# Kernel tuning notes

Hardware: AMD Instinct MI355X
Metric: run time of the kernel (lower is better)

## Reference

```python
import jax, jax.numpy as jnp
import numpy as np

B, T, D = 8, 1024, 1024
KD, VD, H = 1024, 1024, 16  # key_dim_total, value_dim_total, num_heads
NEG = -1e9
EPS = 1e-5


def setup_inputs() -> dict:
    key = jax.random.key(0)
    ks = jax.random.split(key, 8)
    x = jax.random.normal(ks[0], (B, T, D), dtype=jnp.float32)
    x_lens = jax.random.randint(ks[1], (B,), 1, T + 1).astype(jnp.int32)
    ln_gamma = jnp.ones((D,), jnp.float32)
    ln_beta = jnp.zeros((D,), jnp.float32)
    qkv_out = 2 * KD + VD
    w_qkv = jax.random.normal(ks[2], (D, qkv_out), jnp.float32) / np.sqrt(D)
    b_qkv = jax.random.normal(ks[3], (qkv_out,), jnp.float32) * 0.01
    w_out = jax.random.normal(ks[4], (VD, D), jnp.float32) / np.sqrt(VD)
    b_out = jax.random.normal(ks[5], (D,), jnp.float32) * 0.01
    return {"x": x, "x_lens": x_lens, "ln_gamma": ln_gamma, "ln_beta": ln_beta,
            "w_qkv": w_qkv, "b_qkv": b_qkv, "w_out": w_out, "b_out": b_out}


def reference(x, x_lens, ln_gamma, ln_beta, w_qkv, b_qkv, w_out, b_out):
    # LayerNorm over feature dim
    mu = jnp.mean(x, axis=-1, keepdims=True)
    var = jnp.mean(jnp.square(x - mu), axis=-1, keepdims=True)
    xn = (x - mu) * jax.lax.rsqrt(var + EPS) * ln_gamma + ln_beta
    # fused QKV projection
    qkv = xn @ w_qkv + b_qkv  # (B, T, 2*KD+VD)
    q, k, v = qkv[..., :KD], qkv[..., KD:2 * KD], qkv[..., 2 * KD:]
    hd = KD // H
    q = q.reshape(B, T, H, hd).transpose(0, 2, 1, 3)  # (B,H,T,hd)
    k = k.reshape(B, T, H, hd).transpose(0, 2, 1, 3)
    v = v.reshape(B, T, H, VD // H).transpose(0, 2, 1, 3)
    scale = 1.0 / np.sqrt(hd)
    scores = jnp.einsum("bhtd,bhsd->bhts", q, k) * scale  # (B,H,T,T)
    # combined causal + kv-length padding mask (additive in original; boolean here)
    causal = jnp.tril(jnp.ones((T, T), bool))  # (T,T)
    kv_valid = jnp.arange(T)[None, :] < x_lens[:, None]  # (B,T)
    mask = causal[None, None, :, :] & kv_valid[:, None, None, :]
    scores = jnp.where(mask, scores, NEG)
    att = jax.nn.softmax(scores, axis=-1)
    att_out = jnp.einsum("bhts,bhsd->bhtd", att, v)  # (B,H,T,hd_v)
    out = att_out.transpose(0, 2, 1, 3).reshape(B, T, VD)
    out = out @ w_out + b_out
    return out
```

## Files before the change

### kernel.cpp

```cpp
#include <hip/hip_runtime.h>

#define D_MODEL 1024
#define T_SEQ   1024
#define BATCH   8
#define NHEAD   16
#define HDIM    64

typedef float      v4f   __attribute__((ext_vector_type(4)));
typedef _Float16   half8 __attribute__((ext_vector_type(8)));
typedef _Float16   half4h __attribute__((ext_vector_type(4)));
typedef unsigned int ui4 __attribute__((ext_vector_type(4)));

__device__ __forceinline__ void load_lds16(const _Float16* g, _Float16* l) {
  __builtin_amdgcn_global_load_lds(
      (const __attribute__((address_space(1))) unsigned int*)g,
      (__attribute__((address_space(3))) unsigned int*)l, 16, 0, 0);
}

__global__ __launch_bounds__(256) void ln_kernel(const float* __restrict__ x,
                                                 const float* __restrict__ gamma,
                                                 const float* __restrict__ beta,
                                                 _Float16* __restrict__ xn) {
  int row = blockIdx.x;
  int tid = threadIdx.x;
  const float* xr = x + (size_t)row * D_MODEL;
  v4f xv = *(const v4f*)(xr + tid * 4);
  float s  = xv[0] + xv[1] + xv[2] + xv[3];
  float sq = xv[0]*xv[0] + xv[1]*xv[1] + xv[2]*xv[2] + xv[3]*xv[3];
#pragma unroll
  for (int off = 32; off > 0; off >>= 1) {
    s  += __shfl_xor(s, off);
    sq += __shfl_xor(sq, off);
  }
  __shared__ float ps[4], psq[4];
  int wave = tid >> 6;
  if ((tid & 63) == 0) { ps[wave] = s; psq[wave] = sq; }
  __syncthreads();
  float tot  = ps[0] + ps[1] + ps[2] + ps[3];
  float totq = psq[0] + psq[1] + psq[2] + psq[3];
  float mean = tot * (1.0f / D_MODEL);
  float var  = totq * (1.0f / D_MODEL) - mean * mean;
  float rs   = rsqrtf(var + 1e-5f);
  v4f gv = *(const v4f*)(gamma + tid * 4);
  v4f bv = *(const v4f*)(beta + tid * 4);
  half4h o;
#pragma unroll
  for (int i = 0; i < 4; ++i)
    o[i] = (_Float16)((xv[i] - mean) * rs * gv[i] + bv[i]);
  *(half4h*)(xn + (size_t)row * D_MODEL + tid * 4) = o;
}

__global__ __launch_bounds__(256) void fragize_kernel(const float* __restrict__ W,
                                                      _Float16* __restrict__ Bf,
                                                      int N, int K) {
  int g = blockIdx.x * 256 + threadIdx.x;
  int lane = g & 63, tile = g >> 6;
  int ktiles = K >> 5;
  int kt = tile % ktiles, nt = tile / ktiles;
  int n  = nt * 16 + (lane & 15);
  int k0 = kt * 32 + (lane >> 4) * 8;
  half8 o;
#pragma unroll
  for (int j = 0; j < 8; ++j) o[j] = (_Float16)W[(size_t)(k0 + j) * N + n];
  *(half8*)(Bf + (size_t)g * 8) = o;
}

__global__ __launch_bounds__(256) void vtrans_kernel(const _Float16* __restrict__ Vd,
                                                     _Float16* __restrict__ Vt) {
  __shared__ _Float16 tile[64][68];
  int p  = blockIdx.y;
  int t0 = blockIdx.x * 64;
  int tid = threadIdx.x;
  int r = tid >> 3, c = (tid & 7) * 8;
#pragma unroll
  for (int it = 0; it < 2; ++it) {
    int rr = r + it * 32;
    *(ui4*)&tile[rr][c] = *(const ui4*)&Vd[((size_t)p * T_SEQ + t0 + rr) * HDIM + c];
  }
  __syncthreads();
#pragma unroll
  for (int it = 0; it < 2; ++it) {
    int d = r + it * 32;
    half8 o;
#pragma unroll
    for (int j = 0; j < 8; ++j) o[j] = tile[c + j][d];
    *(half8*)&Vt[((size_t)p * HDIM + d) * T_SEQ + t0 + c] = o;
  }
}

template <int MODE>
__global__ __launch_bounds__(256) void gemm_kernel(
    const _Float16* __restrict__ A, const _Float16* __restrict__ Bfrag,
    const float* __restrict__ bias, int M, int N, int K,
    float* __restrict__ outF,
    _Float16* __restrict__ Qd, _Float16* __restrict__ Kd, _Float16* __restrict__ Vd) {
  __shared__ _Float16 As[2][128 * 32];
  int tid = threadIdx.x;
  int wave = tid >> 6, lane = tid & 63;
  int l15 = lane & 15, quad = lane >> 4;
  int wm = (wave & 1) * 64, wn = (wave >> 1) * 64;
  int m0 = blockIdx.x * 128, n0 = blockIdx.y * 128;
  v4f zero = {0.f, 0.f, 0.f, 0.f};
  v4f acc[4][4];
#pragma unroll
  for (int i = 0; i < 4; ++i)
#pragma unroll
    for (int j = 0; j < 4; ++j) acc[i][j] = zero;

  int ar0 = tid >> 2;
  int akc = (tid & 3) * 8;
  const _Float16* Ap = A + (size_t)(m0 + ar0) * K + akc;
  _Float16* AsW0 = &As[0][0] + wave * 512;
  _Float16* AsW1 = &As[1][0] + wave * 512;
  const int ktiles = K >> 5;
  const _Float16* Bp = Bfrag + (size_t)((n0 + wn) >> 4) * ktiles * 512 + lane * 8;

  load_lds16(Ap, AsW0);
  load_lds16(Ap + (size_t)64 * K, AsW0 + 2048);
  for (int kt = 0; kt < ktiles; ++kt) {
    int cur = kt & 1;
    __syncthreads();
    if (kt + 1 < ktiles) {
      _Float16* nx = cur ? AsW0 : AsW1;
      load_lds16(Ap + (kt + 1) * 32,                  nx);
      load_lds16(Ap + (kt + 1) * 32 + (size_t)64 * K, nx + 2048);
    }
    half8 bf[4];
#pragma unroll
    for (int ni = 0; ni < 4; ++ni)
      bf[ni] = *(const half8*)(Bp + ((size_t)ni * ktiles + kt) * 512);
    half8 af[4];
#pragma unroll
    for (int i = 0; i < 4; ++i)
      af[i] = *(const half8*)&As[cur][(wm + i * 16 + l15) * 32 + quad * 8];
#pragma unroll
    for (int mi = 0; mi < 4; ++mi)
#pragma unroll
      for (int ni = 0; ni < 4; ++ni)
        acc[mi][ni] = __builtin_amdgcn_mfma_f32_16x16x32_f16(af[mi], bf[ni], acc[mi][ni], 0, 0, 0);
  }
  float bv[4];
#pragma unroll
  for (int ni = 0; ni < 4; ++ni) bv[ni] = bias[n0 + wn + ni * 16 + l15];
#pragma unroll
  for (int mi = 0; mi < 4; ++mi) {
#pragma unroll
    for (int ni = 0; ni < 4; ++ni) {
      int n = n0 + wn + ni * 16 + l15;
#pragma unroll
      for (int r = 0; r < 4; ++r) {
        int m = m0 + wm + mi * 16 + quad * 4 + r;
        float v = acc[mi][ni][r] + bv[ni];
        if (MODE == 1) {
          outF[(size_t)m * N + n] = v;
        } else {
          int b = m >> 10, t = m & 1023;
          int h = (n >> 6) & 15, d = n & 63;
          size_t idx = ((size_t)(b * NHEAD + h) * T_SEQ + t) * HDIM + d;
          if (n < 1024)        Qd[idx] = (_Float16)(v * 0.18033688f);
          else if (n < 2048)   Kd[idx] = (_Float16)v;
          else                 Vd[idx] = (_Float16)v;
        }
      }
    }
  }
}

__global__ __launch_bounds__(256) void attn_kernel(const _Float16* __restrict__ Qg,
                                                   const _Float16* __restrict__ Kk,
                                                   const _Float16* __restrict__ Vt,
                                                   const int* __restrict__ x_lens,
                                                   _Float16* __restrict__ att) {
  __shared__ _Float16 Ks[2][64 * 32];
  __shared__ _Float16 Vs[2][64 * 32];
  __shared__ _Float16 Pb[4][16 * 72];
  int blk = blockIdx.x;
  int qt = blk >> 7;
  int bh = blk & 127;
  int h  = bh & 15;
  int b  = bh >> 4;
  int t0 = qt * 64;
  int len = x_lens[b];
  int tid = threadIdx.x;
  int wave = tid >> 6, lane = tid & 63;
  int l15 = lane & 15, quad = lane >> 4;
  size_t plane = (size_t)(b * NHEAD + h) * (T_SEQ * HDIM);
  int qrow = t0 + wave * 16;
  int qabs = qrow + l15;
  const _Float16* Qp = Qg + plane + (size_t)qabs * HDIM + quad * 8;
  half8 qf0 = *(const half8*)Qp;
  half8 qf1 = *(const half8*)(Qp + 32);
  v4f zero = {0.f, 0.f, 0.f, 0.f};
  float m_i = -1e30f, l_i = 0.f;
  v4f Ov[4];
#pragma unroll
  for (int nt = 0; nt < 4; ++nt) Ov[nt] = zero;

  int jmaxb = min(t0 + 63, len - 1);
  int ntile = (jmaxb >> 6) + 1;
  int wjmax = min(qrow + 15, len - 1);

  const _Float16* src[4];
  _Float16* dst[4];
  int strd[4];
#pragma unroll
  for (int i = 0; i < 4; ++i) {
    int u = wave * 4 + i;
    int q = u & 3, hf = (u >> 2) & 1;
    if (u < 8) {
      src[i] = Kk + plane + (size_t)(q * 16 + (lane >> 2)) * HDIM + hf * 32 + (lane & 3) * 8;
      dst[i] = &Ks[hf][0] + q * 512;
      strd[i] = 64 * HDIM;
    } else {
      src[i] = Vt + plane + (size_t)(q * 16 + (lane >> 2)) * T_SEQ + hf * 32 + (lane & 3) * 8;
      dst[i] = &Vs[hf][0] + q * 512;
      strd[i] = 64;
    }
  }

  for (int jt = 0; jt < ntile; ++jt) {
    int j0 = jt * 64;
    __syncthreads();
#pragma unroll
    for (int i = 0; i < 4; ++i) {
      load_lds16(src[i], dst[i]);
      src[i] += strd[i];
    }
    __syncthreads();
    if (j0 <= wjmax) {
      v4f s[4];
#pragma unroll
      for (int nt = 0; nt < 4; ++nt) {
        s[nt] = zero;
        half8 k0 = *(const half8*)&Ks[0][(nt * 16 + l15) * 32 + quad * 8];
        half8 k1 = *(const half8*)&Ks[1][(nt * 16 + l15) * 32 + quad * 8];
        s[nt] = __builtin_amdgcn_mfma_f32_16x16x32_f16(k0, qf0, s[nt], 0, 0, 0);
        s[nt] = __builtin_amdgcn_mfma_f32_16x16x32_f16(k1, qf1, s[nt], 0, 0, 0);
      }
      float mnew = m_i;
      bool full = (j0 + 63 <= qrow) && (j0 + 63 < len);
      if (full) {
#pragma unroll
        for (int nt = 0; nt < 4; ++nt)
#pragma unroll
          for (int r = 0; r < 4; ++r)
            mnew = fmaxf(mnew, s[nt][r]);
      } else {
#pragma unroll
        for (int nt = 0; nt < 4; ++nt) {
#pragma unroll
          for (int r = 0; r < 4; ++r) {
            int key = j0 + nt * 16 + quad * 4 + r;
            float v = (key <= qabs && key < len) ? s[nt][r] : -1e30f;
            s[nt][r] = v;
            mnew = fmaxf(mnew, v);
          }
        }
      }
      mnew = fmaxf(mnew, __shfl_xor(mnew, 16));
      mnew = fmaxf(mnew, __shfl_xor(mnew, 32));
      float alpha = exp2f(m_i - mnew);
      m_i = mnew;
      float rsum = 0.f;
#pragma unroll
      for (int nt = 0; nt < 4; ++nt)
#pragma unroll
        for (int r = 0; r < 4; ++r) {
          float p = exp2f(s[nt][r] - mnew);
          s[nt][r] = p;
          rsum += p;
        }
      rsum += __shfl_xor(rsum, 16);
      rsum += __shfl_xor(rsum, 32);
      l_i = l_i * alpha + rsum;
#pragma unroll
      for (int nt = 0; nt < 4; ++nt)
#pragma unroll
        for (int r = 0; r < 4; ++r) Ov[nt][r] *= alpha;
#pragma unroll
      for (int nt = 0; nt < 4; ++nt) {
        half4h pk;
#pragma unroll
        for (int r = 0; r < 4; ++r) pk[r] = (_Float16)s[nt][r];
        *(half4h*)&Pb[wave][l15 * 72 + nt * 16 + quad * 4] = pk;
      }
      asm volatile("s_waitcnt lgkmcnt(0)" ::: "memory");
      half8 pf0 = *(const half8*)&Pb[wave][l15 * 72 + quad * 8];
      half8 pf1 = *(const half8*)&Pb[wave][l15 * 72 + 32 + quad * 8];
#pragma unroll
      for (int nt = 0; nt < 4; ++nt) {
        half8 v0 = *(const half8*)&Vs[0][(nt * 16 + l15) * 32 + quad * 8];
        half8 v1 = *(const half8*)&Vs[1][(nt * 16 + l15) * 32 + quad * 8];
        Ov[nt] = __builtin_amdgcn_mfma_f32_16x16x32_f16(v0, pf0, Ov[nt], 0, 0, 0);
        Ov[nt] = __builtin_amdgcn_mfma_f32_16x16x32_f16(v1, pf1, Ov[nt], 0, 0, 0);
      }
    }
  }
  float inv = 1.0f / l_i;
#pragma unroll
  for (int nt = 0; nt < 4; ++nt) {
    half4h ok;
#pragma unroll
    for (int r = 0; r < 4; ++r) ok[r] = (_Float16)(Ov[nt][r] * inv);
    *(half4h*)&Pb[wave][l15 * 72 + nt * 16 + quad * 4] = ok;
  }
  asm volatile("s_waitcnt lgkmcnt(0)" ::: "memory");
  int r0 = lane >> 3, c0 = (lane & 7) * 8;
  half8 o0 = *(const half8*)&Pb[wave][r0 * 72 + c0];
  half8 o1 = *(const half8*)&Pb[wave][(r0 + 8) * 72 + c0];
  *(half8*)&att[((size_t)(b * T_SEQ) + qrow + r0) * D_MODEL + h * HDIM + c0] = o0;
  *(half8*)&att[((size_t)(b * T_SEQ) + qrow + r0 + 8) * D_MODEL + h * HDIM + c0] = o1;
}

extern "C" void kernel_launch(void* const* d_in, const int* in_sizes, int n_in,
                              void* d_out, int out_size, void* d_ws, size_t ws_size,
                              hipStream_t stream) {
  const float* x        = (const float*)d_in[0];
  const int*   x_lens   = (const int*)d_in[1];
  const float* ln_gamma = (const float*)d_in[2];
  const float* ln_beta  = (const float*)d_in[3];
  const float* w_qkv    = (const float*)d_in[4];
  const float* b_qkv    = (const float*)d_in[5];
  const float* w_out    = (const float*)d_in[6];
  const float* b_out    = (const float*)d_in[7];
  float* out = (float*)d_out;

  char* w = (char*)d_ws;
  _Float16* xn    = (_Float16*)w; w += (size_t)8192 * 1024 * 2;
  _Float16* BfQKV = (_Float16*)w; w += (size_t)3072 * 1024 * 2;
  _Float16* BfOut = (_Float16*)w; w += (size_t)1024 * 1024 * 2;
  _Float16* Qd    = (_Float16*)w; w += (size_t)8192 * 1024 * 2;
  _Float16* Kd    = (_Float16*)w; w += (size_t)8192 * 1024 * 2;
  _Float16* Vd    = (_Float16*)w; w += (size_t)8192 * 1024 * 2;
  _Float16* att   = (_Float16*)w; w += (size_t)8192 * 1024 * 2;
  _Float16* Vt    = xn;

  fragize_kernel<<<(3072 * 1024 / 8) / 256, 256, 0, stream>>>(w_qkv, BfQKV, 3072, 1024);
  fragize_kernel<<<(1024 * 1024 / 8) / 256, 256, 0, stream>>>(w_out, BfOut, 1024, 1024);
  ln_kernel<<<8192, 256, 0, stream>>>(x, ln_gamma, ln_beta, xn);
  gemm_kernel<0><<<dim3(8192 / 128, 3072 / 128), 256, 0, stream>>>(
      xn, BfQKV, b_qkv, 8192, 3072, 1024, nullptr, Qd, Kd, Vd);
  vtrans_kernel<<<dim3(16, 128), 256, 0, stream>>>(Vd, Vt);
  attn_kernel<<<2048, 256, 0, stream>>>(Qd, Kd, Vt, x_lens, att);
  gemm_kernel<1><<<dim3(8192 / 128, 1024 / 128), 256, 0, stream>>>(
      att, BfOut, b_out, 8192, 1024, 1024, out, nullptr, nullptr, nullptr);
}
```

Baseline: 254.0 us.

## Replace QKV GEMM with 128x256-tile, 8-wave pipelined kernel using transposed weights

Swaps the QKV projection GEMM for a new 512-thread kernel that computes 128x256 output tiles. Both operands are staged through double-buffered, XOR-swizzled LDS with direct global-to-LDS loads, and MFMA phases are interleaved with barriers and wave priority changes. The weight is now pre-transposed into a K-contiguous fp16 layout by a new tiled transpose kernel, replacing the fragment layout. This aims to raise data reuse and overlap loads with MFMA, at the cost of higher LDS use, more barriers, and scattered scalar fp16 stores in the epilogue.

```diff
diff --git a/kernel.cpp b/kernel.cpp
--- a/kernel.cpp
+++ b/kernel.cpp
@@ -65,6 +65,35 @@
   *(half8*)(Bf + (size_t)g * 8) = o;
 }
 
+__global__ __launch_bounds__(256) void wtrans_kernel(const float* __restrict__ W,
+                                                     _Float16* __restrict__ Wt,
+                                                     int N, int K) {
+  __shared__ _Float16 t[64][72];
+  int k0 = blockIdx.x * 64, n0 = blockIdx.y * 64;
+  int tid = threadIdx.x;
+  int r = tid >> 3, c = (tid & 7) * 8;
+#pragma unroll
+  for (int it = 0; it < 2; ++it) {
+    int row = r + it * 32;
+    const float* src = W + (size_t)(k0 + row) * N + n0 + c;
+    v4f x0 = *(const v4f*)src;
+    v4f x1 = *(const v4f*)(src + 4);
+#pragma unroll
+    for (int j = 0; j < 4; ++j) t[row][c + j] = (_Float16)x0[j];
+#pragma unroll
+    for (int j = 0; j < 4; ++j) t[row][c + 4 + j] = (_Float16)x1[j];
+  }
+  __syncthreads();
+#pragma unroll
+  for (int it = 0; it < 2; ++it) {
+    int d = r + it * 32;
+    half8 o;
+#pragma unroll
+    for (int j = 0; j < 8; ++j) o[j] = t[c + j][d];
+    *(half8*)(Wt + (size_t)(n0 + d) * K + k0 + c) = o;
+  }
+}
+
 __global__ __launch_bounds__(256) void vtrans_kernel(const _Float16* __restrict__ Vd,
                                                      _Float16* __restrict__ Vt) {
   __shared__ _Float16 tile[64][68];
@@ -86,6 +115,124 @@
     for (int j = 0; j < 8; ++j) o[j] = tile[c + j][d];
     *(half8*)&Vt[((size_t)p * HDIM + d) * T_SEQ + t0 + c] = o;
   }
+}
+
+
+#define BAR   __builtin_amdgcn_s_barrier()
+#define LGKM0 asm volatile("s_waitcnt lgkmcnt(0)" ::: "memory")
+#define VMC2  asm volatile("s_waitcnt vmcnt(2)" ::: "memory")
+#define PRIO1 __builtin_amdgcn_s_setprio(1)
+#define PRIO0 __builtin_amdgcn_s_setprio(0)
+
+#define RDA(dst, BUF, KK)                                                       \
+  _Pragma("unroll")                                                             \
+  for (int d2 = 0; d2 < 4; ++d2)                                                \
+    dst[d2] = *(const half8*)(lds + (BUF) +                                     \
+                              (wm + d2 * 16 + l15) * 64 +                       \
+                              ((((KK) * 4 + quad) ^ swz) * 8));
+
+#define RDB(dst, BUF, NI0, KK)                                                  \
+  _Pragma("unroll")                                                             \
+  for (int n2 = 0; n2 < 2; ++n2)                                                \
+    dst[n2] = *(const half8*)(lds + (BUF) + 8192 +                              \
+                              (wn + ((NI0) + n2) * 16 + l15) * 64 +             \
+                              ((((KK) * 4 + quad) ^ swz) * 8));
+
+#define MFQ(A_, B_, NI0)                                                        \
+  _Pragma("unroll")                                                             \
+  for (int mi = 0; mi < 4; ++mi)                                                \
+    _Pragma("unroll")                                                           \
+    for (int n2 = 0; n2 < 2; ++n2)                                              \
+      acc[mi][(NI0) + n2] = __builtin_amdgcn_mfma_f32_16x16x32_f16(             \
+          A_[mi], B_[n2], acc[mi][(NI0) + n2], 0, 0, 0);
+
+#define STGA(BUF, R0, KT)                                                       \
+  load_lds16(Asrc + (size_t)(R0) * 1024 + (KT) * 64, ldst + (BUF) + (R0) * 64)
+#define STGB(BUF, R0, KT)                                                       \
+  load_lds16(Bsrc + (size_t)(R0) * 1024 + (KT) * 64, ldst + (BUF) + 8192 + (R0) * 64)
+
+__global__ __launch_bounds__(512, 2) void gemm256_qkv(
+    const _Float16* __restrict__ A, const _Float16* __restrict__ Bt,
+    const float* __restrict__ bias,
+    _Float16* __restrict__ Qd, _Float16* __restrict__ Kd, _Float16* __restrict__ Vd) {
+  __shared__ _Float16 lds[49152];
+  const int K = 1024;
+  int tid  = threadIdx.x;
+  int wave = tid >> 6, lane = tid & 63;
+  int l15  = lane & 15, quad = lane >> 4;
+  int wm = (wave & 1) * 64, wn = (wave >> 1) * 64;
+  int m0 = blockIdx.x * 128, n0 = blockIdx.y * 256;
+  int swz = l15 & 7;
+
+  int ric = tid >> 3;
+  int colofs = ((tid & 7) ^ (ric & 7)) * 8;
+  const _Float16* Asrc = A  + (size_t)(m0 + ric) * K + colofs;
+  const _Float16* Bsrc = Bt + (size_t)(n0 + ric) * K + colofs;
+  _Float16* ldst = lds + wave * 512;
+
+  const int B0 = 0, B1 = 24576;
+  v4f acc[4][4];
+  v4f zero = {0.f, 0.f, 0.f, 0.f};
+#pragma unroll
+  for (int i = 0; i < 4; ++i)
+#pragma unroll
+    for (int j = 0; j < 4; ++j) acc[i][j] = zero;
+
+  STGA(B0, 0, 0); STGA(B0, 64, 0);
+  STGB(B0, 0, 0); STGB(B0, 64, 0); STGB(B0, 128, 0); STGB(B0, 192, 0);
+  STGA(B1, 0, 1); STGA(B1, 64, 1);
+  VMC2; BAR;
+
+  half8 a0[4], a1[4], bl[2], bh[2];
+#pragma unroll 1
+  for (int i = 0; i < 8; ++i) {
+    int kt1 = 2 * i + 1;
+    int kt2 = (2 * i + 2 < 16) ? 2 * i + 2 : 15;
+    int kt3 = (2 * i + 3 < 16) ? 2 * i + 3 : 15;
+    RDA(a0, B0, 0); RDB(bl, B0, 0, 0);
+    STGB(B1, 0, kt1); STGB(B1, 64, kt1);
+    BAR; LGKM0; PRIO1; MFQ(a0, bl, 0); PRIO0; BAR;
+    RDB(bh, B0, 2, 0);
+    STGB(B1, 128, kt1); STGB(B1, 192, kt1);
+    BAR; LGKM0; PRIO1; MFQ(a0, bh, 2); PRIO0; BAR;
+    RDA(a1, B0, 1); RDB(bl, B0, 0, 1);
+    BAR; LGKM0; PRIO1; MFQ(a1, bl, 0); PRIO0; BAR;
+    RDB(bh, B0, 2, 1);
+    STGA(B0, 0, kt2); STGA(B0, 64, kt2);
+    VMC2; BAR; LGKM0; PRIO1; MFQ(a1, bh, 2); PRIO0; BAR;
+    RDA(a0, B1, 0); RDB(bl, B1, 0, 0);
+    STGB(B0, 0, kt2); STGB(B0, 64, kt2);
+    BAR; LGKM0; PRIO1; MFQ(a0, bl, 0); PRIO0; BAR;
+    RDB(bh, B1, 2, 0);
+    STGB(B0, 128, kt2); STGB(B0, 192, kt2);
+    BAR; LGKM0; PRIO1; MFQ(a0, bh, 2); PRIO0; BAR;
+    RDA(a1, B1, 1); RDB(bl, B1, 0, 1);
+    BAR; LGKM0; PRIO1; MFQ(a1, bl, 0); PRIO0; BAR;
+    RDB(bh, B1, 2, 1);
+    STGA(B1, 0, kt3); STGA(B1, 64, kt3);
+    VMC2; BAR; LGKM0; PRIO1; MFQ(a1, bh, 2); PRIO0; BAR;
+  }
+
+  float bv[4];
+#pragma unroll
+  for (int ni = 0; ni < 4; ++ni) bv[ni] = bias[n0 + wn + ni * 16 + l15];
+  int sec = n0 >> 10;
+  _Float16* dstP = sec == 0 ? Qd : (sec == 1 ? Kd : Vd);
+  float scale = sec == 0 ? 0.18033688f : 1.0f;
+#pragma unroll
+  for (int mi = 0; mi < 4; ++mi)
+#pragma unroll
+    for (int ni = 0; ni < 4; ++ni) {
+      int n = n0 + wn + ni * 16 + l15;
+      int h = (n >> 6) & 15, d = n & 63;
+#pragma unroll
+      for (int r = 0; r < 4; ++r) {
+        int m = m0 + wm + mi * 16 + quad * 4 + r;
+        int b = m >> 10, t = m & 1023;
+        float v = acc[mi][ni][r] + bv[ni];
+        dstP[((size_t)(b * NHEAD + h) * T_SEQ + t) * HDIM + d] = (_Float16)(v * scale);
+      }
+    }
 }
 
 template <int MODE>
@@ -327,7 +474,7 @@
 
   char* w = (char*)d_ws;
   _Float16* xn    = (_Float16*)w; w += (size_t)8192 * 1024 * 2;
-  _Float16* BfQKV = (_Float16*)w; w += (size_t)3072 * 1024 * 2;
+  _Float16* WtQKV = (_Float16*)w; w += (size_t)3072 * 1024 * 2;
   _Float16* BfOut = (_Float16*)w; w += (size_t)1024 * 1024 * 2;
   _Float16* Qd    = (_Float16*)w; w += (size_t)8192 * 1024 * 2;
   _Float16* Kd    = (_Float16*)w; w += (size_t)8192 * 1024 * 2;
@@ -335,11 +482,10 @@
   _Float16* att   = (_Float16*)w; w += (size_t)8192 * 1024 * 2;
   _Float16* Vt    = xn;
 
-  fragize_kernel<<<(3072 * 1024 / 8) / 256, 256, 0, stream>>>(w_qkv, BfQKV, 3072, 1024);
+  wtrans_kernel<<<dim3(16, 48), 256, 0, stream>>>(w_qkv, WtQKV, 3072, 1024);
   fragize_kernel<<<(1024 * 1024 / 8) / 256, 256, 0, stream>>>(w_out, BfOut, 1024, 1024);
   ln_kernel<<<8192, 256, 0, stream>>>(x, ln_gamma, ln_beta, xn);
-  gemm_kernel<0><<<dim3(8192 / 128, 3072 / 128), 256, 0, stream>>>(
-      xn, BfQKV, b_qkv, 8192, 3072, 1024, nullptr, Qd, Kd, Vd);
+  gemm256_qkv<<<dim3(64, 12), 512, 0, stream>>>(xn, WtQKV, b_qkv, Qd, Kd, Vd);
   vtrans_kernel<<<dim3(16, 128), 256, 0, stream>>>(Vd, Vt);
   attn_kernel<<<2048, 256, 0, stream>>>(Qd, Kd, Vt, x_lens, att);
   gemm_kernel<1><<<dim3(8192 / 128, 1024 / 128), 256, 0, stream>>>(
```

New measurement: 246.0 us. 3.1% less time.

## Double-buffer K/V tiles in attention and schedule heaviest query tiles first

Applied to the files above, without the earlier changes.

Attention K/V tiles now use two LDS buffers, so the next tile's global-to-LDS load is issued before computing on the current one, with vmcnt waits replacing the pair of full syncthreads. Query tiles are launched in reverse order so the longest causal blocks start first, and MFMA sections are wrapped with s_setprio to favour matrix issue. This hides load latency at the cost of double the K/V LDS, which may lower occupancy.

```diff
diff --git a/kernel.cpp b/kernel.cpp
--- a/kernel.cpp
+++ b/kernel.cpp
@@ -171,11 +171,11 @@
                                                    const _Float16* __restrict__ Vt,
                                                    const int* __restrict__ x_lens,
                                                    _Float16* __restrict__ att) {
-  __shared__ _Float16 Ks[2][64 * 32];
-  __shared__ _Float16 Vs[2][64 * 32];
+  __shared__ _Float16 Ks[2][2][2048];
+  __shared__ _Float16 Vs[2][2][2048];
   __shared__ _Float16 Pb[4][16 * 72];
   int blk = blockIdx.x;
-  int qt = blk >> 7;
+  int qt = 15 - (blk >> 7);
   int bh = blk & 127;
   int h  = bh & 15;
   int b  = bh >> 4;
@@ -201,7 +201,7 @@
   int wjmax = min(qrow + 15, len - 1);
 
   const _Float16* src[4];
-  _Float16* dst[4];
+  _Float16* dst0[4];
   int strd[4];
 #pragma unroll
   for (int i = 0; i < 4; ++i) {
@@ -209,34 +209,46 @@
     int q = u & 3, hf = (u >> 2) & 1;
     if (u < 8) {
       src[i] = Kk + plane + (size_t)(q * 16 + (lane >> 2)) * HDIM + hf * 32 + (lane & 3) * 8;
-      dst[i] = &Ks[hf][0] + q * 512;
+      dst0[i] = &Ks[0][hf][0] + q * 512;
       strd[i] = 64 * HDIM;
     } else {
       src[i] = Vt + plane + (size_t)(q * 16 + (lane >> 2)) * T_SEQ + hf * 32 + (lane & 3) * 8;
-      dst[i] = &Vs[hf][0] + q * 512;
+      dst0[i] = &Vs[0][hf][0] + q * 512;
       strd[i] = 64;
     }
   }
+
+#pragma unroll
+  for (int i = 0; i < 4; ++i) { load_lds16(src[i], dst0[i]); src[i] += strd[i]; }
 
   for (int jt = 0; jt < ntile; ++jt) {
     int j0 = jt * 64;
-    __syncthreads();
-#pragma unroll
-    for (int i = 0; i < 4; ++i) {
-      load_lds16(src[i], dst[i]);
-      src[i] += strd[i];
-    }
-    __syncthreads();
+    int cur = jt & 1;
+    __builtin_amdgcn_s_barrier();
+    if (jt + 1 < ntile) {
+#pragma unroll
+      for (int i = 0; i < 4; ++i) {
+        load_lds16(src[i], dst0[i] + (cur ^ 1) * 4096);
+        src[i] += strd[i];
+      }
+      asm volatile("s_waitcnt vmcnt(4)" ::: "memory");
+    } else {
+      asm volatile("s_waitcnt vmcnt(0)" ::: "memory");
+    }
+    __builtin_amdgcn_s_barrier();
+    __builtin_amdgcn_sched_barrier(0);
     if (j0 <= wjmax) {
       v4f s[4];
+      __builtin_amdgcn_s_setprio(1);
 #pragma unroll
       for (int nt = 0; nt < 4; ++nt) {
         s[nt] = zero;
-        half8 k0 = *(const half8*)&Ks[0][(nt * 16 + l15) * 32 + quad * 8];
-        half8 k1 = *(const half8*)&Ks[1][(nt * 16 + l15) * 32 + quad * 8];
+        half8 k0 = *(const half8*)&Ks[cur][0][(nt * 16 + l15) * 32 + quad * 8];
+        half8 k1 = *(const half8*)&Ks[cur][1][(nt * 16 + l15) * 32 + quad * 8];
         s[nt] = __builtin_amdgcn_mfma_f32_16x16x32_f16(k0, qf0, s[nt], 0, 0, 0);
         s[nt] = __builtin_amdgcn_mfma_f32_16x16x32_f16(k1, qf1, s[nt], 0, 0, 0);
       }
+      __builtin_amdgcn_s_setprio(0);
       float mnew = m_i;
       bool full = (j0 + 63 <= qrow) && (j0 + 63 < len);
       if (full) {
@@ -287,13 +299,15 @@
       asm volatile("s_waitcnt lgkmcnt(0)" ::: "memory");
       half8 pf0 = *(const half8*)&Pb[wave][l15 * 72 + quad * 8];
       half8 pf1 = *(const half8*)&Pb[wave][l15 * 72 + 32 + quad * 8];
+      __builtin_amdgcn_s_setprio(1);
 #pragma unroll
       for (int nt = 0; nt < 4; ++nt) {
-        half8 v0 = *(const half8*)&Vs[0][(nt * 16 + l15) * 32 + quad * 8];
-        half8 v1 = *(const half8*)&Vs[1][(nt * 16 + l15) * 32 + quad * 8];
+        half8 v0 = *(const half8*)&Vs[cur][0][(nt * 16 + l15) * 32 + quad * 8];
+        half8 v1 = *(const half8*)&Vs[cur][1][(nt * 16 + l15) * 32 + quad * 8];
         Ov[nt] = __builtin_amdgcn_mfma_f32_16x16x32_f16(v0, pf0, Ov[nt], 0, 0, 0);
         Ov[nt] = __builtin_amdgcn_mfma_f32_16x16x32_f16(v1, pf1, Ov[nt], 0, 0, 0);
       }
+      __builtin_amdgcn_s_setprio(0);
     }
   }
   float inv = 1.0f / l_i;
```

Measured after the change: 247.5 us. 2.5% less time.
